# Kernel tuning notes

Hardware: AMD Instinct MI355X
Metric: run time of the kernel (lower is better)

## Reference

```python
import jax, jax.numpy as jnp
import numpy as np


def setup_inputs() -> dict:
    key = jax.random.key(0)
    B, C, H, W = 16, 64, 256, 256
    inp = jax.random.normal(key, (B, C, H, W), dtype=jnp.float32)
    return {"input": inp, "k": 512}


def reference(input, k):
    B, C, H, W = input.shape
    flat = input.reshape(B, C, H * W)            # [B, C, HW]
    heatmap = flat[:, 0]                          # [B, HW]
    _, idx = jax.lax.top_k(heatmap, k)            # [B, k], sorted descending like torch.topk

    # gather features for all channels at the top-k spatial locations
    gather_idx = jnp.broadcast_to(idx[:, None, :], (B, C, k))
    features = jnp.take_along_axis(flat, gather_idx, axis=2)  # [B, C, k]

    # normalized grid coordinates: x in [-1,1] left->right, y in [1,-1] top->bottom
    xs = jnp.linspace(-1.0, 1.0, W, dtype=input.dtype)
    ys = jnp.linspace(1.0, -1.0, H, dtype=input.dtype)
    col = idx % W
    row = idx // W
    x_loc = xs[col]                               # [B, k]
    y_loc = ys[row]                               # [B, k]
    location = jnp.stack((x_loc, y_loc), axis=1)  # [B, 2, k]
    return (features, location)
```

## Files before the change

### kernel.cpp

```cpp
#include <hip/hip_runtime.h>

#define HWSZ 65536
#define WDIM 256
#define NB   16
#define NC   64
#define TOPK 512
#define NBINS 4096
#define CAP  2048

__device__ __forceinline__ unsigned key32(float v) {
    unsigned u = __float_as_uint(v);
    return (u & 0x80000000u) ? ~u : (u | 0x80000000u);
}

__global__ void zero_kernel(int* hist, int* cnt) {
    int i = blockIdx.x * 1024 + threadIdx.x;
    if (i < NB * NBINS) hist[i] = 0;
    if (i < NB) cnt[i] = 0;
}

__global__ __launch_bounds__(1024) void hist_kernel(const float* __restrict__ in,
                                                    int* __restrict__ hist) {
    __shared__ int lh[NBINS];
    int b = blockIdx.y;
    for (int i = threadIdx.x; i < NBINS; i += 1024) lh[i] = 0;
    __syncthreads();
    const float4* hm = (const float4*)(in + (size_t)b * NC * HWSZ);
    int base = blockIdx.x * (HWSZ / 4 / 4);
#pragma unroll
    for (int t = 0; t < (HWSZ / 4 / 4) / 1024; ++t) {
        float4 v = hm[base + t * 1024 + threadIdx.x];
        atomicAdd(&lh[key32(v.x) >> 20], 1);
        atomicAdd(&lh[key32(v.y) >> 20], 1);
        atomicAdd(&lh[key32(v.z) >> 20], 1);
        atomicAdd(&lh[key32(v.w) >> 20], 1);
    }
    __syncthreads();
    for (int i = threadIdx.x; i < NBINS; i += 1024) {
        int c = lh[i];
        if (c) atomicAdd(&hist[b * NBINS + i], c);
    }
}

__global__ __launch_bounds__(1024) void findbin_kernel(const int* __restrict__ hist,
                                                       int* __restrict__ dstar) {
    __shared__ int ps[1024];
    int b = blockIdx.x, t = threadIdx.x;
    const int* hb = hist + b * NBINS;
    int h0 = hb[4 * t + 0], h1 = hb[4 * t + 1], h2 = hb[4 * t + 2], h3 = hb[4 * t + 3];
    ps[t] = h0 + h1 + h2 + h3;
    __syncthreads();
    for (int off = 1; off < 1024; off <<= 1) {
        int add = (t + off < 1024) ? ps[t + off] : 0;
        __syncthreads();
        ps[t] += add;
        __syncthreads();
    }
    int S = ps[t];
    int Snext = (t < 1023) ? ps[t + 1] : 0;
    if (S >= TOPK && Snext < TOPK) {
        int d;
        if (Snext + h3 >= TOPK) d = 4 * t + 3;
        else if (Snext + h3 + h2 >= TOPK) d = 4 * t + 2;
        else if (Snext + h3 + h2 + h1 >= TOPK) d = 4 * t + 1;
        else d = 4 * t;
        dstar[b] = d;
    }
}

__global__ __launch_bounds__(1024) void collect_kernel(const float* __restrict__ in,
                                                       const int* __restrict__ dstar,
                                                       int* __restrict__ cnt,
                                                       unsigned long long* __restrict__ cand) {
    int b = blockIdx.y;
    unsigned thresh = (unsigned)dstar[b] << 20;
    const float4* hm = (const float4*)(in + (size_t)b * NC * HWSZ);
    int base = blockIdx.x * (HWSZ / 4 / 4);
#pragma unroll
    for (int t = 0; t < (HWSZ / 4 / 4) / 1024; ++t) {
        int i4 = base + t * 1024 + threadIdx.x;
        float4 v = hm[i4];
        float vv[4] = {v.x, v.y, v.z, v.w};
#pragma unroll
        for (int e = 0; e < 4; ++e) {
            unsigned kk = key32(vv[e]);
            if (kk >= thresh) {
                int i = i4 * 4 + e;
                int pos = atomicAdd(&cnt[b], 1);
                if (pos < CAP)
                    cand[(size_t)b * CAP + pos] =
                        ((unsigned long long)kk << 32) | (unsigned)(~i);
            }
        }
    }
}

__global__ __launch_bounds__(1024) void sort_kernel(const unsigned long long* __restrict__ cand,
                                                    const int* __restrict__ cnt,
                                                    int* __restrict__ idx_out,
                                                    float* __restrict__ out) {
    __shared__ unsigned long long s[CAP];
    int b = blockIdx.x, t = threadIdx.x;
    int n = cnt[b];
    if (n > CAP) n = CAP;
    for (int i = t; i < CAP; i += 1024)
        s[i] = (i < n) ? ~cand[(size_t)b * CAP + i] : 0xFFFFFFFFFFFFFFFFull;
    __syncthreads();
    for (int ksz = 2; ksz <= CAP; ksz <<= 1) {
        for (int j = ksz >> 1; j > 0; j >>= 1) {
            for (int i = t; i < CAP; i += 1024) {
                int ixj = i ^ j;
                if (ixj > i) {
                    unsigned long long a = s[i], c = s[ixj];
                    bool up = ((i & ksz) == 0);
                    if ((a > c) == up) { s[i] = c; s[ixj] = a; }
                }
            }
            __syncthreads();
        }
    }
    if (t < TOPK) {
        unsigned long long comp = ~s[t];
        unsigned low = (unsigned)comp;
        int idx = (int)(~low) & 0xFFFF;
        idx_out[b * TOPK + t] = idx;
        int col = idx & (WDIM - 1);
        int row = idx >> 8;
        float x = -1.0f + col * (2.0f / 255.0f);
        float y = 1.0f - row * (2.0f / 255.0f);
        float* loc = out + (size_t)NB * NC * TOPK;
        loc[(b * 2 + 0) * TOPK + t] = x;
        loc[(b * 2 + 1) * TOPK + t] = y;
    }
}

__global__ void gather_kernel(const float* __restrict__ in,
                              const int* __restrict__ idx,
                              float* __restrict__ out) {
    int b = blockIdx.y, c = blockIdx.x, t = threadIdx.x;
    int gi = idx[b * TOPK + t] & 0xFFFF;
    out[((size_t)b * NC + c) * TOPK + t] = in[((size_t)b * NC + c) * HWSZ + gi];
}

extern "C" void kernel_launch(void* const* d_in, const int* in_sizes, int n_in,
                              void* d_out, int out_size, void* d_ws, size_t ws_size,
                              hipStream_t stream) {
    const float* in = (const float*)d_in[0];
    float* out = (float*)d_out;

    char* ws = (char*)d_ws;
    int* hist = (int*)(ws);
    int* cnt  = (int*)(ws + 262144);
    int* dstar = (int*)(ws + 262144 + 64);
    int* idxb = (int*)(ws + 262272);
    unsigned long long* cand = (unsigned long long*)(ws + 295040);

    zero_kernel<<<(NB * NBINS + 1023) / 1024, 1024, 0, stream>>>(hist, cnt);
    hist_kernel<<<dim3(4, NB), 1024, 0, stream>>>(in, hist);
    findbin_kernel<<<NB, 1024, 0, stream>>>(hist, dstar);
    collect_kernel<<<dim3(4, NB), 1024, 0, stream>>>(in, dstar, cnt, cand);
    sort_kernel<<<NB, 1024, 0, stream>>>(cand, cnt, idxb, out);
    gather_kernel<<<dim3(NC, NB), TOPK, 0, stream>>>(in, idxb, out);
}
```

Before: 449.0 us.

## Fuse histogram reduction into collect, drop zero kernel, shrink candidate sort

Each histogram block now writes its per-chunk histogram to a slab instead of issuing global atomics, so the zero kernel goes away. The collect kernel sums the chunk histograms and finds the threshold bin itself, which removes the separate findbin launch. The grid grows from 4 to 8 chunks per batch for more parallelism. The candidate cap is halved to 1024 so the bitonic sort needs one element per thread, at the risk of dropping candidates when ties in the threshold bin push the count past 1024.

```diff
diff --git a/kernel.cpp b/kernel.cpp
--- a/kernel.cpp
+++ b/kernel.cpp
@@ -6,29 +6,26 @@
 #define NC   64
 #define TOPK 512
 #define NBINS 4096
-#define CAP  2048
+#define NCHUNK 8
+#define CAP  1024
 
 __device__ __forceinline__ unsigned key32(float v) {
     unsigned u = __float_as_uint(v);
     return (u & 0x80000000u) ? ~u : (u | 0x80000000u);
 }
 
-__global__ void zero_kernel(int* hist, int* cnt) {
-    int i = blockIdx.x * 1024 + threadIdx.x;
-    if (i < NB * NBINS) hist[i] = 0;
-    if (i < NB) cnt[i] = 0;
-}
-
 __global__ __launch_bounds__(1024) void hist_kernel(const float* __restrict__ in,
-                                                    int* __restrict__ hist) {
+                                                    int* __restrict__ slab,
+                                                    int* __restrict__ cnt) {
     __shared__ int lh[NBINS];
-    int b = blockIdx.y;
+    int b = blockIdx.y, chunk = blockIdx.x;
     for (int i = threadIdx.x; i < NBINS; i += 1024) lh[i] = 0;
+    if (chunk == 0 && threadIdx.x == 0) cnt[b] = 0;
     __syncthreads();
     const float4* hm = (const float4*)(in + (size_t)b * NC * HWSZ);
-    int base = blockIdx.x * (HWSZ / 4 / 4);
+    int base = chunk * (HWSZ / NCHUNK / 4);
 #pragma unroll
-    for (int t = 0; t < (HWSZ / 4 / 4) / 1024; ++t) {
+    for (int t = 0; t < (HWSZ / NCHUNK / 4) / 1024; ++t) {
         float4 v = hm[base + t * 1024 + threadIdx.x];
         atomicAdd(&lh[key32(v.x) >> 20], 1);
         atomicAdd(&lh[key32(v.y) >> 20], 1);
@@ -36,18 +33,26 @@
         atomicAdd(&lh[key32(v.w) >> 20], 1);
     }
     __syncthreads();
-    for (int i = threadIdx.x; i < NBINS; i += 1024) {
-        int c = lh[i];
-        if (c) atomicAdd(&hist[b * NBINS + i], c);
-    }
+    int* dst = slab + ((size_t)b * NCHUNK + chunk) * NBINS;
+    for (int i = threadIdx.x; i < NBINS; i += 1024) dst[i] = lh[i];
 }
 
-__global__ __launch_bounds__(1024) void findbin_kernel(const int* __restrict__ hist,
-                                                       int* __restrict__ dstar) {
+__global__ __launch_bounds__(1024) void collect_kernel(const float* __restrict__ in,
+                                                       const int* __restrict__ slab,
+                                                       int* __restrict__ cnt,
+                                                       unsigned long long* __restrict__ cand,
+                                                       int* __restrict__ dstar_dbg) {
     __shared__ int ps[1024];
-    int b = blockIdx.x, t = threadIdx.x;
-    const int* hb = hist + b * NBINS;
-    int h0 = hb[4 * t + 0], h1 = hb[4 * t + 1], h2 = hb[4 * t + 2], h3 = hb[4 * t + 3];
+    __shared__ int sh_dstar;
+    int b = blockIdx.y, chunk = blockIdx.x, t = threadIdx.x;
+
+    const int* sb = slab + (size_t)b * NCHUNK * NBINS;
+    int h0 = 0, h1 = 0, h2 = 0, h3 = 0;
+#pragma unroll
+    for (int c = 0; c < NCHUNK; ++c) {
+        const int* s4 = sb + c * NBINS + 4 * t;
+        h0 += s4[0]; h1 += s4[1]; h2 += s4[2]; h3 += s4[3];
+    }
     ps[t] = h0 + h1 + h2 + h3;
     __syncthreads();
     for (int off = 1; off < 1024; off <<= 1) {
@@ -64,21 +69,17 @@
         else if (Snext + h3 + h2 >= TOPK) d = 4 * t + 2;
         else if (Snext + h3 + h2 + h1 >= TOPK) d = 4 * t + 1;
         else d = 4 * t;
-        dstar[b] = d;
+        sh_dstar = d;
+        if (chunk == 0) dstar_dbg[b] = d;
     }
-}
+    __syncthreads();
+    unsigned thresh = (unsigned)sh_dstar << 20;
 
-__global__ __launch_bounds__(1024) void collect_kernel(const float* __restrict__ in,
-                                                       const int* __restrict__ dstar,
-                                                       int* __restrict__ cnt,
-                                                       unsigned long long* __restrict__ cand) {
-    int b = blockIdx.y;
-    unsigned thresh = (unsigned)dstar[b] << 20;
     const float4* hm = (const float4*)(in + (size_t)b * NC * HWSZ);
-    int base = blockIdx.x * (HWSZ / 4 / 4);
+    int base = chunk * (HWSZ / NCHUNK / 4);
 #pragma unroll
-    for (int t = 0; t < (HWSZ / 4 / 4) / 1024; ++t) {
-        int i4 = base + t * 1024 + threadIdx.x;
+    for (int u = 0; u < (HWSZ / NCHUNK / 4) / 1024; ++u) {
+        int i4 = base + u * 1024 + t;
         float4 v = hm[i4];
         float vv[4] = {v.x, v.y, v.z, v.w};
 #pragma unroll
@@ -103,18 +104,15 @@
     int b = blockIdx.x, t = threadIdx.x;
     int n = cnt[b];
     if (n > CAP) n = CAP;
-    for (int i = t; i < CAP; i += 1024)
-        s[i] = (i < n) ? ~cand[(size_t)b * CAP + i] : 0xFFFFFFFFFFFFFFFFull;
+    s[t] = (t < n) ? ~cand[(size_t)b * CAP + t] : 0xFFFFFFFFFFFFFFFFull;
     __syncthreads();
     for (int ksz = 2; ksz <= CAP; ksz <<= 1) {
         for (int j = ksz >> 1; j > 0; j >>= 1) {
-            for (int i = t; i < CAP; i += 1024) {
-                int ixj = i ^ j;
-                if (ixj > i) {
-                    unsigned long long a = s[i], c = s[ixj];
-                    bool up = ((i & ksz) == 0);
-                    if ((a > c) == up) { s[i] = c; s[ixj] = a; }
-                }
+            int ixj = t ^ j;
+            if (ixj > t) {
+                unsigned long long a = s[t], c = s[ixj];
+                bool up = ((t & ksz) == 0);
+                if ((a > c) == up) { s[t] = c; s[ixj] = a; }
             }
             __syncthreads();
         }
@@ -149,16 +147,14 @@
     float* out = (float*)d_out;
 
     char* ws = (char*)d_ws;
-    int* hist = (int*)(ws);
-    int* cnt  = (int*)(ws + 262144);
-    int* dstar = (int*)(ws + 262144 + 64);
-    int* idxb = (int*)(ws + 262272);
-    unsigned long long* cand = (unsigned long long*)(ws + 295040);
+    int* slab = (int*)(ws);
+    int* cnt  = (int*)(ws + 2097152);
+    int* dstar = (int*)(ws + 2097152 + 64);
+    int* idxb = (int*)(ws + 2097280);
+    unsigned long long* cand = (unsigned long long*)(ws + 2130048);
 
-    zero_kernel<<<(NB * NBINS + 1023) / 1024, 1024, 0, stream>>>(hist, cnt);
-    hist_kernel<<<dim3(4, NB), 1024, 0, stream>>>(in, hist);
-    findbin_kernel<<<NB, 1024, 0, stream>>>(hist, dstar);
-    collect_kernel<<<dim3(4, NB), 1024, 0, stream>>>(in, dstar, cnt, cand);
+    hist_kernel<<<dim3(NCHUNK, NB), 1024, 0, stream>>>(in, slab, cnt);
+    collect_kernel<<<dim3(NCHUNK, NB), 1024, 0, stream>>>(in, slab, cnt, cand, dstar);
     sort_kernel<<<NB, 1024, 0, stream>>>(cand, cnt, idxb, out);
     gather_kernel<<<dim3(NC, NB), TOPK, 0, stream>>>(in, idxb, out);
 }
```

Measured after the change: 430.3 us. -4.2%, faster.
